# Kernel optimization log

Hardware: AMD Instinct MI355X
Metric: run time of the kernel (lower is better)

The kernel has to match this reference:

```python
import jax, jax.numpy as jnp
import numpy as np

IGNORE_INDEX = -100
LABEL_SMOOTHING = 0.0


def setup_inputs() -> dict:
    key = jax.random.key(0)
    k1, k2, k3, k4 = jax.random.split(key, 4)
    BT, H, V = 4096, 1024, 32000
    x = jax.random.normal(k1, (BT, H), dtype=jnp.float32)
    target = jax.random.randint(k2, (BT,), 0, V, dtype=jnp.int64)
    # scale weight so logits have O(1) std (realistic trained lm_head scale)
    weight = jax.random.normal(k3, (V, H), dtype=jnp.float32) * 0.02
    bias = jax.random.normal(k4, (V,), dtype=jnp.float32) * 0.02
    return {"x": x, "target": target, "weight": weight, "bias": bias}


def reference(x, target, weight, bias):
    # x: [BT, H], weight: [V, H], bias: [V], target: [BT]
    V = weight.shape[0]
    ls = LABEL_SMOOTHING
    logits = x @ weight.T + bias                     # [BT, V]
    lse = jax.nn.logsumexp(logits, axis=-1)          # [BT]
    # gather logit at the target class (clip so ignore_index rows stay in-bounds)
    safe_t = jnp.clip(target, 0, V - 1)
    x_y = jnp.take_along_axis(logits, safe_t[:, None], axis=-1)[:, 0]
    # CE with label smoothing: (1-ls)*(lse - x_y) + ls*lse - (ls/V)*sum_j x_j
    per_row = (1.0 - ls) * (lse - x_y)
    if ls > 0.0:
        per_row = per_row + ls * lse - (ls / V) * jnp.sum(logits, axis=-1)
    valid = target != IGNORE_INDEX
    per_row = jnp.where(valid, per_row, 0.0)
    n_non_ignore = jnp.sum(valid).astype(per_row.dtype)
    loss = jnp.sum(per_row) / n_non_ignore
    return loss
```

## Files before the change

### kernel.cpp

```cpp
#include <hip/hip_runtime.h>
#include <hip/hip_bf16.h>
#include <stdint.h>


typedef float f16v __attribute__((ext_vector_type(16)));
typedef int v8i __attribute__((ext_vector_type(8)));

__device__ __forceinline__ unsigned pk_fp8(float4 v) {
  int w = 0;
  w = __builtin_amdgcn_cvt_pk_fp8_f32(v.x, v.y, w, false);
  w = __builtin_amdgcn_cvt_pk_fp8_f32(v.z, v.w, w, true);
  return (unsigned)w;
}

__global__ __launch_bounds__(256) void cast_swz_k(const float* __restrict__ in,
                                                  uint4* __restrict__ out,
                                                  long n16) {
  long t = (long)blockIdx.x * blockDim.x + threadIdx.x;
  long stride = (long)gridDim.x * blockDim.x;
  for (; t < n16; t += stride) {
    long o = t * 16;
    int c = (int)(o >> 11);
    int rem = (int)(o & 2047);
    int h = rem >> 10;
    int lam = (rem >> 4) & 63;
    int row = (c >> 4) * 32 + (lam & 31);
    int k = (c & 15) * 64 + (lam >> 5) * 32 + h * 16;
    const float4* src = (const float4*)(in + (long)row * 1024 + k);
    uint4 oo;
    oo.x = pk_fp8(src[0]); oo.y = pk_fp8(src[1]);
    oo.z = pk_fp8(src[2]); oo.w = pk_fp8(src[3]);
    out[t] = oo;
  }
}

__global__ __launch_bounds__(256) void xy_k(const float* __restrict__ x,
                                            const float* __restrict__ w,
                                            const float* __restrict__ bias,
                                            const int* __restrict__ tgt,
                                            float* __restrict__ xy, int H, int V) {
  int row = blockIdx.x;
  int t = tgt[row];
  int st = min(max(t, 0), V - 1);
  const float4* xr = (const float4*)(x + (long)row * H);
  const float4* wr = (const float4*)(w + (long)st * H);
  float s = 0.f;
  int n4 = H >> 2;
  for (int i = threadIdx.x; i < n4; i += 256) {
    float4 a = xr[i], b = wr[i];
    s += a.x * b.x + a.y * b.y + a.z * b.z + a.w * b.w;
  }
  for (int off = 32; off; off >>= 1) s += __shfl_down(s, off, 64);
  __shared__ float sm[4];
  if ((threadIdx.x & 63) == 0) sm[threadIdx.x >> 6] = s;
  __syncthreads();
  if (threadIdx.x == 0) xy[row] = sm[0] + sm[1] + sm[2] + sm[3] + bias[st];
}

#define LDS_BUF 24576

__global__ __launch_bounds__(256, 2)
void gemm_sumexp(const char* __restrict__ Xf, const char* __restrict__ Wf,
                 const float* __restrict__ bias, float* __restrict__ partials,
                 int H, int BT) {
  __shared__ char lds[2 * LDS_BUF];
  __shared__ float rowsum[2][256];

  const int tid = threadIdx.x;
  const int w = tid >> 6, lane = tid & 63;
  const int wr = w >> 1, wc = w & 1;
  const int l32 = lane & 31, kh = lane >> 5;

  const int nbx = gridDim.x;
  const int nwg = nbx * gridDim.y;
  const int id = blockIdx.y * nbx + blockIdx.x;
  const int swz = ((nwg & 7) == 0) ? ((id & 7) * (nwg >> 3) + (id >> 3)) : id;
  const int bx = swz % nbx;
  const int by = swz / nbx;
  const int m0 = bx * 256, n0 = by * 128;

  const char* segsrc[6];
  int segdst[6];
#pragma unroll
  for (int r = 0; r < 6; ++r) {
    const int s = w * 6 + r;
    if (s < 16) {
      long base = (long)(bx * 8 + (s >> 1)) * 32768 + (long)(s & 1) * 1024;
      segsrc[r] = Xf + base + lane * 16;
    } else {
      long base = (long)(by * 4 + ((s - 16) >> 1)) * 32768 + (long)((s - 16) & 1) * 1024;
      segsrc[r] = Wf + base + lane * 16;
    }
    segdst[r] = s * 1024;
  }

  auto STAGE = [&](int g) {
    const int bo = (g & 1) * LDS_BUF;
#pragma unroll
    for (int r = 0; r < 6; ++r)
      __builtin_amdgcn_global_load_lds(
          (const __attribute__((address_space(1))) void*)(segsrc[r] + (long)g * 2048),
          (__attribute__((address_space(3))) void*)(lds + bo + segdst[r]),
          16, 0, 0);
  };

  f16v acc[4][2];
#pragma unroll
  for (int mi = 0; mi < 4; mi++)
#pragma unroll
    for (int ni = 0; ni < 2; ni++)
#pragma unroll
      for (int r = 0; r < 16; r++) acc[mi][ni][r] = 0.f;

  const int nG = H >> 6;

  STAGE(0);
  STAGE(1);
  asm volatile("s_waitcnt vmcnt(6)" ::: "memory");
  __builtin_amdgcn_s_barrier();

#pragma unroll 2
  for (int g = 0; g < nG; ++g) {
    const int bo = (g & 1) * LDS_BUF;
    v8i a[4], b[2];
#pragma unroll
    for (int mi = 0; mi < 4; mi++) {
      const char* p = lds + bo + (wr * 4 + mi) * 2048 + lane * 16;
      int4 lo = *(const int4*)(p);
      int4 hi = *(const int4*)(p + 1024);
      v8i t;
      t[0] = lo.x; t[1] = lo.y; t[2] = lo.z; t[3] = lo.w;
      t[4] = hi.x; t[5] = hi.y; t[6] = hi.z; t[7] = hi.w;
      a[mi] = t;
    }
#pragma unroll
    for (int ni = 0; ni < 2; ni++) {
      const char* p = lds + bo + 16384 + (wc * 2 + ni) * 2048 + lane * 16;
      int4 lo = *(const int4*)(p);
      int4 hi = *(const int4*)(p + 1024);
      v8i t;
      t[0] = lo.x; t[1] = lo.y; t[2] = lo.z; t[3] = lo.w;
      t[4] = hi.x; t[5] = hi.y; t[6] = hi.z; t[7] = hi.w;
      b[ni] = t;
    }
    __builtin_amdgcn_s_setprio(1);
#pragma unroll
    for (int mi = 0; mi < 4; mi++)
#pragma unroll
      for (int ni = 0; ni < 2; ni++)
        acc[mi][ni] = __builtin_amdgcn_mfma_scale_f32_32x32x64_f8f6f4(
            a[mi], b[ni], acc[mi][ni], 0 , 0 ,
            0, 127 , 0, 127 );
    __builtin_amdgcn_s_setprio(0);

    __builtin_amdgcn_s_barrier();
    if (g + 2 < nG) {
      STAGE(g + 2);
      asm volatile("s_waitcnt vmcnt(6)" ::: "memory");
    } else {
      asm volatile("s_waitcnt vmcnt(0)" ::: "memory");
    }
    __builtin_amdgcn_s_barrier();
  }

  float bv[2];
  bv[0] = bias[n0 + wc * 64 + l32];
  bv[1] = bias[n0 + wc * 64 + 32 + l32];

#pragma unroll
  for (int mi = 0; mi < 4; mi++) {
    float p[16];
#pragma unroll
    for (int r = 0; r < 16; r++) p[r] = 0.f;
#pragma unroll
    for (int ni = 0; ni < 2; ni++)
#pragma unroll
      for (int r = 0; r < 16; r++) p[r] += __expf(acc[mi][ni][r] + bv[ni]);
#pragma unroll
    for (int off = 1; off < 32; off <<= 1)
#pragma unroll
      for (int r = 0; r < 16; r++) p[r] += __shfl_xor(p[r], off, 32);
    if (l32 == 0) {
#pragma unroll
      for (int r = 0; r < 16; r++)
        rowsum[wc][wr * 128 + mi * 32 + (r & 3) + 8 * (r >> 2) + 4 * kh] = p[r];
    }
  }
  __syncthreads();
  partials[(long)by * BT + m0 + tid] = rowsum[0][tid] + rowsum[1][tid];
}

__global__ __launch_bounds__(256)
void row_reduce(const float* __restrict__ partials, const float* __restrict__ xy,
                const int* __restrict__ tgt, float* __restrict__ bsum,
                float* __restrict__ bcnt, int BT, int nCB) {
  const int row = blockIdx.x * 64 + (threadIdx.x >> 2);
  const int q = threadIdx.x & 3;
  float S = 0.f;
  for (int b = q; b < nCB; b += 4) S += partials[(long)b * BT + row];
  S += __shfl_xor(S, 1, 64);
  S += __shfl_xor(S, 2, 64);
  float pr = 0.f, c = 0.f;
  if (q == 0) {
    int t = tgt[row];
    if (t != -100) { pr = logf(S) - xy[row]; c = 1.f; }
  }
  for (int off = 32; off; off >>= 1) {
    pr += __shfl_down(pr, off, 64);
    c += __shfl_down(c, off, 64);
  }
  __shared__ float sp[4], sc[4];
  if ((threadIdx.x & 63) == 0) {
    sp[threadIdx.x >> 6] = pr;
    sc[threadIdx.x >> 6] = c;
  }
  __syncthreads();
  if (threadIdx.x == 0) {
    bsum[blockIdx.x] = sp[0] + sp[1] + sp[2] + sp[3];
    bcnt[blockIdx.x] = sc[0] + sc[1] + sc[2] + sc[3];
  }
}

__global__ void finalize(const float* __restrict__ bsum, const float* __restrict__ bcnt,
                         float* __restrict__ out, int nb) {
  float s = 0.f, c = 0.f;
  for (int i = threadIdx.x; i < nb; i += 64) { s += bsum[i]; c += bcnt[i]; }
  for (int off = 32; off; off >>= 1) {
    s += __shfl_down(s, off, 64);
    c += __shfl_down(c, off, 64);
  }
  if (threadIdx.x == 0) out[0] = s / c;
}

extern "C" void kernel_launch(void* const* d_in, const int* in_sizes, int n_in,
                              void* d_out, int out_size, void* d_ws, size_t ws_size,
                              hipStream_t stream) {
  const float* x = (const float*)d_in[0];
  const int* tgt = (const int*)d_in[1];
  const float* w = (const float*)d_in[2];
  const float* bias = (const float*)d_in[3];
  float* out = (float*)d_out;

  const int BT = in_sizes[1];
  const int V = in_sizes[3];
  const int H = in_sizes[0] / BT;
  const int nCB = V / 128;

  char* ws = (char*)d_ws;
  const long wb_bytes = (long)V * H;
  const long xb_bytes = (long)BT * H;
  char* Wf = ws;
  char* Xf = ws + wb_bytes;
  float* partials = (float*)(ws + wb_bytes + xb_bytes);
  float* xy = partials + (long)nCB * BT;
  float* bsum = xy + BT;
  float* bcnt = bsum + (BT / 64);

  cast_swz_k<<<8192, 256, 0, stream>>>(w, (uint4*)Wf, (long)V * H / 16);
  cast_swz_k<<<1024, 256, 0, stream>>>(x, (uint4*)Xf, (long)BT * H / 16);
  xy_k<<<BT, 256, 0, stream>>>(x, w, bias, tgt, xy, H, V);
  dim3 grid(BT / 256, nCB);
  gemm_sumexp<<<grid, 256, 0, stream>>>(Xf, Wf, bias, partials, H, BT);
  row_reduce<<<BT / 64, 256, 0, stream>>>(partials, xy, tgt, bsum, bcnt, BT, nCB);
  finalize<<<1, 64, 0, stream>>>(bsum, bcnt, out, BT / 64);
}
```

Baseline: 389.9 us.

## Widen GEMM tile to 256x256 with 8 waves and triple-buffered interleaved prefetch

The fp8 GEMM+sumexp kernel now uses 512 threads per block and a 256x256 output tile, which halves the number of column blocks and improves operand reuse. LDS goes from a double buffer to a triple buffer, and global-to-LDS loads are split into four chunks that are issued between groups of MFMAs inside each k-step. The aim is to hide load latency and cut redundant reads of X. The cost is more barriers per iteration and higher LDS use (about 100KB), which may limit occupancy to one block per CU despite the launch bound of 2.

```diff
diff --git a/kernel.cpp b/kernel.cpp
--- a/kernel.cpp
+++ b/kernel.cpp
@@ -57,18 +57,18 @@
   if (threadIdx.x == 0) xy[row] = sm[0] + sm[1] + sm[2] + sm[3] + bias[st];
 }
 
-#define LDS_BUF 24576
-
-__global__ __launch_bounds__(256, 2)
+#define LDS_KG 32768
+
+__global__ __launch_bounds__(512, 2)
 void gemm_sumexp(const char* __restrict__ Xf, const char* __restrict__ Wf,
                  const float* __restrict__ bias, float* __restrict__ partials,
                  int H, int BT) {
-  __shared__ char lds[2 * LDS_BUF];
-  __shared__ float rowsum[2][256];
+  __shared__ char lds[3 * LDS_KG];
+  __shared__ float rowsum[4][256];
 
   const int tid = threadIdx.x;
   const int w = tid >> 6, lane = tid & 63;
-  const int wr = w >> 1, wc = w & 1;
+  const int wr = w >> 2, wc = w & 3;
   const int l32 = lane & 31, kh = lane >> 5;
 
   const int nbx = gridDim.x;
@@ -77,31 +77,28 @@
   const int swz = ((nwg & 7) == 0) ? ((id & 7) * (nwg >> 3) + (id >> 3)) : id;
   const int bx = swz % nbx;
   const int by = swz / nbx;
-  const int m0 = bx * 256, n0 = by * 128;
-
-  const char* segsrc[6];
-  int segdst[6];
-#pragma unroll
-  for (int r = 0; r < 6; ++r) {
-    const int s = w * 6 + r;
+  const int m0 = bx * 256, n0 = by * 256;
+
+  const char* segsrc[4];
+  int segdst[4];
+#pragma unroll
+  for (int r = 0; r < 4; ++r) {
+    const int s = w * 4 + r;
     if (s < 16) {
       long base = (long)(bx * 8 + (s >> 1)) * 32768 + (long)(s & 1) * 1024;
       segsrc[r] = Xf + base + lane * 16;
     } else {
-      long base = (long)(by * 4 + ((s - 16) >> 1)) * 32768 + (long)((s - 16) & 1) * 1024;
+      long base = (long)(by * 8 + ((s - 16) >> 1)) * 32768 + (long)((s - 16) & 1) * 1024;
       segsrc[r] = Wf + base + lane * 16;
     }
     segdst[r] = s * 1024;
   }
 
-  auto STAGE = [&](int g) {
-    const int bo = (g & 1) * LDS_BUF;
-#pragma unroll
-    for (int r = 0; r < 6; ++r)
-      __builtin_amdgcn_global_load_lds(
-          (const __attribute__((address_space(1))) void*)(segsrc[r] + (long)g * 2048),
-          (__attribute__((address_space(3))) void*)(lds + bo + segdst[r]),
-          16, 0, 0);
+  auto STAGE1 = [&](int g, int bo, int r) {
+    __builtin_amdgcn_global_load_lds(
+        (const __attribute__((address_space(1))) void*)(segsrc[r] + (long)g * 2048),
+        (__attribute__((address_space(3))) void*)(lds + bo + segdst[r]),
+        16, 0, 0);
   };
 
   f16v acc[4][2];
@@ -114,53 +111,89 @@
 
   const int nG = H >> 6;
 
-  STAGE(0);
-  STAGE(1);
-  asm volatile("s_waitcnt vmcnt(6)" ::: "memory");
+  {
+#pragma unroll
+    for (int r = 0; r < 4; ++r) STAGE1(0, 0, r);
+#pragma unroll
+    for (int r = 0; r < 4; ++r) STAGE1(1, LDS_KG, r);
+  }
+  asm volatile("s_waitcnt vmcnt(4)" ::: "memory");
   __builtin_amdgcn_s_barrier();
 
-#pragma unroll 2
+  int bo = 0;
   for (int g = 0; g < nG; ++g) {
-    const int bo = (g & 1) * LDS_BUF;
-    v8i a[4], b[2];
-#pragma unroll
-    for (int mi = 0; mi < 4; mi++) {
-      const char* p = lds + bo + (wr * 4 + mi) * 2048 + lane * 16;
-      int4 lo = *(const int4*)(p);
-      int4 hi = *(const int4*)(p + 1024);
-      v8i t;
-      t[0] = lo.x; t[1] = lo.y; t[2] = lo.z; t[3] = lo.w;
-      t[4] = hi.x; t[5] = hi.y; t[6] = hi.z; t[7] = hi.w;
-      a[mi] = t;
+    const char* A = lds + bo;
+    const char* B = lds + bo + 16384;
+    int bo2 = bo + 2 * LDS_KG;
+    if (bo2 >= 3 * LDS_KG) bo2 -= 3 * LDS_KG;
+    const bool pf = (g + 2 < nG);
+
+    v8i a0, a1, a2, a3, b0, b1;
+#define LDFRAG(dst, base, chunk)                                   \
+    {                                                              \
+      const char* p = (base) + (chunk) * 2048 + lane * 16;         \
+      int4 lo = *(const int4*)(p);                                 \
+      int4 hi = *(const int4*)(p + 1024);                          \
+      v8i t;                                                       \
+      t[0] = lo.x; t[1] = lo.y; t[2] = lo.z; t[3] = lo.w;          \
+      t[4] = hi.x; t[5] = hi.y; t[6] = hi.z; t[7] = hi.w;          \
+      dst = t;                                                     \
     }
-#pragma unroll
-    for (int ni = 0; ni < 2; ni++) {
-      const char* p = lds + bo + 16384 + (wc * 2 + ni) * 2048 + lane * 16;
-      int4 lo = *(const int4*)(p);
-      int4 hi = *(const int4*)(p + 1024);
-      v8i t;
-      t[0] = lo.x; t[1] = lo.y; t[2] = lo.z; t[3] = lo.w;
-      t[4] = hi.x; t[5] = hi.y; t[6] = hi.z; t[7] = hi.w;
-      b[ni] = t;
-    }
+
+    LDFRAG(a0, A, (wr * 4 + 0));
+    LDFRAG(a1, A, (wr * 4 + 1));
+    LDFRAG(b0, B, (wc * 2 + 0));
+    if (pf) STAGE1(g + 2, bo2, 0);
+    __builtin_amdgcn_s_barrier();
     __builtin_amdgcn_s_setprio(1);
-#pragma unroll
-    for (int mi = 0; mi < 4; mi++)
-#pragma unroll
-      for (int ni = 0; ni < 2; ni++)
-        acc[mi][ni] = __builtin_amdgcn_mfma_scale_f32_32x32x64_f8f6f4(
-            a[mi], b[ni], acc[mi][ni], 0 , 0 ,
-            0, 127 , 0, 127 );
+    acc[0][0] = __builtin_amdgcn_mfma_scale_f32_32x32x64_f8f6f4(
+        a0, b0, acc[0][0], 0, 0, 0, 127, 0, 127);
+    acc[1][0] = __builtin_amdgcn_mfma_scale_f32_32x32x64_f8f6f4(
+        a1, b0, acc[1][0], 0, 0, 0, 127, 0, 127);
     __builtin_amdgcn_s_setprio(0);
-
-    __builtin_amdgcn_s_barrier();
-    if (g + 2 < nG) {
-      STAGE(g + 2);
-      asm volatile("s_waitcnt vmcnt(6)" ::: "memory");
-    } else {
+    __builtin_amdgcn_s_barrier();
+
+    LDFRAG(a2, A, (wr * 4 + 2));
+    LDFRAG(a3, A, (wr * 4 + 3));
+    LDFRAG(b1, B, (wc * 2 + 1));
+    if (pf) STAGE1(g + 2, bo2, 1);
+    __builtin_amdgcn_s_barrier();
+    __builtin_amdgcn_s_setprio(1);
+    acc[2][0] = __builtin_amdgcn_mfma_scale_f32_32x32x64_f8f6f4(
+        a2, b0, acc[2][0], 0, 0, 0, 127, 0, 127);
+    acc[3][0] = __builtin_amdgcn_mfma_scale_f32_32x32x64_f8f6f4(
+        a3, b0, acc[3][0], 0, 0, 0, 127, 0, 127);
+    __builtin_amdgcn_s_setprio(0);
+    __builtin_amdgcn_s_barrier();
+
+    if (pf) STAGE1(g + 2, bo2, 2);
+    __builtin_amdgcn_s_barrier();
+    __builtin_amdgcn_s_setprio(1);
+    acc[0][1] = __builtin_amdgcn_mfma_scale_f32_32x32x64_f8f6f4(
+        a0, b1, acc[0][1], 0, 0, 0, 127, 0, 127);
+    acc[1][1] = __builtin_amdgcn_mfma_scale_f32_32x32x64_f8f6f4(
+        a1, b1, acc[1][1], 0, 0, 0, 127, 0, 127);
+    __builtin_amdgcn_s_setprio(0);
+    __builtin_amdgcn_s_barrier();
+
+    if (pf) STAGE1(g + 2, bo2, 3);
+    __builtin_amdgcn_s_barrier();
+    __builtin_amdgcn_s_setprio(1);
+    acc[2][1] = __builtin_amdgcn_mfma_scale_f32_32x32x64_f8f6f4(
+        a2, b1, acc[2][1], 0, 0, 0, 127, 0, 127);
+    acc[3][1] = __builtin_amdgcn_mfma_scale_f32_32x32x64_f8f6f4(
+        a3, b1, acc[3][1], 0, 0, 0, 127, 0, 127);
+    __builtin_amdgcn_s_setprio(0);
+    if (pf) {
+      asm volatile("s_waitcnt vmcnt(4)" ::: "memory");
+    } else if (g + 1 < nG) {
       asm volatile("s_waitcnt vmcnt(0)" ::: "memory");
     }
     __builtin_amdgcn_s_barrier();
+
+    bo += LDS_KG;
+    if (bo >= 3 * LDS_KG) bo -= 3 * LDS_KG;
+#undef LDFRAG
   }
 
   float bv[2];
@@ -187,7 +220,9 @@
     }
   }
   __syncthreads();
-  partials[(long)by * BT + m0 + tid] = rowsum[0][tid] + rowsum[1][tid];
+  if (tid < 256)
+    partials[(long)by * BT + m0 + tid] =
+        rowsum[0][tid] + rowsum[1][tid] + rowsum[2][tid] + rowsum[3][tid];
 }
 
 __global__ __launch_bounds__(256)
@@ -244,7 +279,7 @@
   const int BT = in_sizes[1];
   const int V = in_sizes[3];
   const int H = in_sizes[0] / BT;
-  const int nCB = V / 128;
+  const int nCB = V / 256;
 
   char* ws = (char*)d_ws;
   const long wb_bytes = (long)V * H;
@@ -260,7 +295,7 @@
   cast_swz_k<<<1024, 256, 0, stream>>>(x, (uint4*)Xf, (long)BT * H / 16);
   xy_k<<<BT, 256, 0, stream>>>(x, w, bias, tgt, xy, H, V);
   dim3 grid(BT / 256, nCB);
-  gemm_sumexp<<<grid, 256, 0, stream>>>(Xf, Wf, bias, partials, H, BT);
+  gemm_sumexp<<<grid, 512, 0, stream>>>(Xf, Wf, bias, partials, H, BT);
   row_reduce<<<BT / 64, 256, 0, stream>>>(partials, xy, tgt, bsum, bcnt, BT, nCB);
   finalize<<<1, 64, 0, stream>>>(bsum, bcnt, out, BT / 64);
 }
```

After: 423.5 us. 8.6% more time.

## Load MFMA fragments directly from global into registers, bypassing LDS staging

Applied to the files above, without the earlier changes.

The fp8 cast kernel now lays out each 32-row by 64-k chunk so that every lane's 32-byte MFMA fragment is contiguous. The GEMM then drops LDS double-buffering and its barriers, loading each wave's operands straight from global memory into registers with a two-step register prefetch. This removes LDS traffic and block-wide synchronisation. In exchange, operand tiles shared across waves are no longer reused through LDS, so waves sharing a row or column block fetch the same data from global/L2 separately. It also raises register pressure.

```diff
diff --git a/kernel.cpp b/kernel.cpp
--- a/kernel.cpp
+++ b/kernel.cpp
@@ -5,6 +5,7 @@
 
 typedef float f16v __attribute__((ext_vector_type(16)));
 typedef int v8i __attribute__((ext_vector_type(8)));
+typedef int v4i __attribute__((ext_vector_type(4)));
 
 __device__ __forceinline__ unsigned pk_fp8(float4 v) {
   int w = 0;
@@ -22,10 +23,10 @@
     long o = t * 16;
     int c = (int)(o >> 11);
     int rem = (int)(o & 2047);
-    int h = rem >> 10;
-    int lam = (rem >> 4) & 63;
-    int row = (c >> 4) * 32 + (lam & 31);
-    int k = (c & 15) * 64 + (lam >> 5) * 32 + h * 16;
+    int l = rem >> 5;
+    int b0 = rem & 31;
+    int row = (c >> 4) * 32 + (l & 31);
+    int k = (c & 15) * 64 + (l >> 5) * 32 + b0;
     const float4* src = (const float4*)(in + (long)row * 1024 + k);
     uint4 oo;
     oo.x = pk_fp8(src[0]); oo.y = pk_fp8(src[1]);
@@ -57,13 +58,17 @@
   if (threadIdx.x == 0) xy[row] = sm[0] + sm[1] + sm[2] + sm[3] + bias[st];
 }
 
-#define LDS_BUF 24576
+__device__ __forceinline__ v8i ldfrag(const char* p) {
+  const v4i* q = (const v4i*)p;
+  v4i lo = q[0];
+  v4i hi = q[1];
+  return __builtin_shufflevector(lo, hi, 0, 1, 2, 3, 4, 5, 6, 7);
+}
 
 __global__ __launch_bounds__(256, 2)
 void gemm_sumexp(const char* __restrict__ Xf, const char* __restrict__ Wf,
                  const float* __restrict__ bias, float* __restrict__ partials,
                  int H, int BT) {
-  __shared__ char lds[2 * LDS_BUF];
   __shared__ float rowsum[2][256];
 
   const int tid = threadIdx.x;
@@ -79,89 +84,67 @@
   const int by = swz / nbx;
   const int m0 = bx * 256, n0 = by * 128;
 
-  const char* segsrc[6];
-  int segdst[6];
-#pragma unroll
-  for (int r = 0; r < 6; ++r) {
-    const int s = w * 6 + r;
-    if (s < 16) {
-      long base = (long)(bx * 8 + (s >> 1)) * 32768 + (long)(s & 1) * 1024;
-      segsrc[r] = Xf + base + lane * 16;
-    } else {
-      long base = (long)(by * 4 + ((s - 16) >> 1)) * 32768 + (long)((s - 16) & 1) * 1024;
-      segsrc[r] = Wf + base + lane * 16;
+  const int Rb = bx * 8 + wr * 4;
+  const int Nb = by * 4 + wc * 2;
+
+  const char* pf[6];
+#pragma unroll
+  for (int mi = 0; mi < 4; mi++)
+    pf[mi] = Xf + (long)(Rb + mi) * 32768 + lane * 32;
+#pragma unroll
+  for (int ni = 0; ni < 2; ni++)
+    pf[4 + ni] = Wf + (long)(Nb + ni) * 32768 + lane * 32;
+
+  f16v acc[4][2];
+#pragma unroll
+  for (int mi = 0; mi < 4; mi++)
+#pragma unroll
+    for (int ni = 0; ni < 2; ni++)
+#pragma unroll
+      for (int r = 0; r < 16; r++) acc[mi][ni][r] = 0.f;
+
+  const int nG = H >> 6;
+
+  v8i cur[6], nxt[6];
+#pragma unroll
+  for (int i = 0; i < 6; i++) cur[i] = ldfrag(pf[i]);
+
+#define MFMA_BATCH(OPS)                                                       \
+  {                                                                           \
+    acc[0][0] = __builtin_amdgcn_mfma_scale_f32_32x32x64_f8f6f4(              \
+        OPS[0], OPS[4], acc[0][0], 0, 0, 0, 127, 0, 127);                     \
+    acc[1][0] = __builtin_amdgcn_mfma_scale_f32_32x32x64_f8f6f4(              \
+        OPS[1], OPS[4], acc[1][0], 0, 0, 0, 127, 0, 127);                     \
+    acc[2][0] = __builtin_amdgcn_mfma_scale_f32_32x32x64_f8f6f4(              \
+        OPS[2], OPS[4], acc[2][0], 0, 0, 0, 127, 0, 127);                     \
+    acc[3][0] = __builtin_amdgcn_mfma_scale_f32_32x32x64_f8f6f4(              \
+        OPS[3], OPS[4], acc[3][0], 0, 0, 0, 127, 0, 127);                     \
+    acc[0][1] = __builtin_amdgcn_mfma_scale_f32_32x32x64_f8f6f4(              \
+        OPS[0], OPS[5], acc[0][1], 0, 0, 0, 127, 0, 127);                     \
+    acc[1][1] = __builtin_amdgcn_mfma_scale_f32_32x32x64_f8f6f4(              \
+        OPS[1], OPS[5], acc[1][1], 0, 0, 0, 127, 0, 127);                     \
+    acc[2][1] = __builtin_amdgcn_mfma_scale_f32_32x32x64_f8f6f4(              \
+        OPS[2], OPS[5], acc[2][1], 0, 0, 0, 127, 0, 127);                     \
+    acc[3][1] = __builtin_amdgcn_mfma_scale_f32_32x32x64_f8f6f4(              \
+        OPS[3], OPS[5], acc[3][1], 0, 0, 0, 127, 0, 127);                     \
+  }
+
+#pragma unroll 1
+  for (int g = 0; g + 2 <= nG; g += 2) {
+    {
+      const long ko = (long)(g + 1) * 2048;
+#pragma unroll
+      for (int i = 0; i < 6; i++) nxt[i] = ldfrag(pf[i] + ko);
     }
-    segdst[r] = s * 1024;
-  }
-
-  auto STAGE = [&](int g) {
-    const int bo = (g & 1) * LDS_BUF;
-#pragma unroll
-    for (int r = 0; r < 6; ++r)
-      __builtin_amdgcn_global_load_lds(
-          (const __attribute__((address_space(1))) void*)(segsrc[r] + (long)g * 2048),
-          (__attribute__((address_space(3))) void*)(lds + bo + segdst[r]),
-          16, 0, 0);
-  };
-
-  f16v acc[4][2];
-#pragma unroll
-  for (int mi = 0; mi < 4; mi++)
-#pragma unroll
-    for (int ni = 0; ni < 2; ni++)
-#pragma unroll
-      for (int r = 0; r < 16; r++) acc[mi][ni][r] = 0.f;
-
-  const int nG = H >> 6;
-
-  STAGE(0);
-  STAGE(1);
-  asm volatile("s_waitcnt vmcnt(6)" ::: "memory");
-  __builtin_amdgcn_s_barrier();
-
-#pragma unroll 2
-  for (int g = 0; g < nG; ++g) {
-    const int bo = (g & 1) * LDS_BUF;
-    v8i a[4], b[2];
-#pragma unroll
-    for (int mi = 0; mi < 4; mi++) {
-      const char* p = lds + bo + (wr * 4 + mi) * 2048 + lane * 16;
-      int4 lo = *(const int4*)(p);
-      int4 hi = *(const int4*)(p + 1024);
-      v8i t;
-      t[0] = lo.x; t[1] = lo.y; t[2] = lo.z; t[3] = lo.w;
-      t[4] = hi.x; t[5] = hi.y; t[6] = hi.z; t[7] = hi.w;
-      a[mi] = t;
+    MFMA_BATCH(cur);
+    if (g + 2 < nG) {
+      const long ko = (long)(g + 2) * 2048;
+#pragma unroll
+      for (int i = 0; i < 6; i++) cur[i] = ldfrag(pf[i] + ko);
     }
-#pragma unroll
-    for (int ni = 0; ni < 2; ni++) {
-      const char* p = lds + bo + 16384 + (wc * 2 + ni) * 2048 + lane * 16;
-      int4 lo = *(const int4*)(p);
-      int4 hi = *(const int4*)(p + 1024);
-      v8i t;
-      t[0] = lo.x; t[1] = lo.y; t[2] = lo.z; t[3] = lo.w;
-      t[4] = hi.x; t[5] = hi.y; t[6] = hi.z; t[7] = hi.w;
-      b[ni] = t;
-    }
-    __builtin_amdgcn_s_setprio(1);
-#pragma unroll
-    for (int mi = 0; mi < 4; mi++)
-#pragma unroll
-      for (int ni = 0; ni < 2; ni++)
-        acc[mi][ni] = __builtin_amdgcn_mfma_scale_f32_32x32x64_f8f6f4(
-            a[mi], b[ni], acc[mi][ni], 0 , 0 ,
-            0, 127 , 0, 127 );
-    __builtin_amdgcn_s_setprio(0);
-
-    __builtin_amdgcn_s_barrier();
-    if (g + 2 < nG) {
-      STAGE(g + 2);
-      asm volatile("s_waitcnt vmcnt(6)" ::: "memory");
-    } else {
-      asm volatile("s_waitcnt vmcnt(0)" ::: "memory");
-    }
-    __builtin_amdgcn_s_barrier();
-  }
+    MFMA_BATCH(nxt);
+  }
+#undef MFMA_BATCH
 
   float bv[2];
   bv[0] = bias[n0 + wc * 64 + l32];
```

Result: slower. 635.0 us (+62.9%).
